# Kernel optimization log

Hardware: AMD Instinct MI355X
Metric: run time of the kernel (lower is better)

## Reference

```python
import jax, jax.numpy as jnp
import numpy as np

B, T, D = 4, 1024, 2048
H = 32
HD = D // H  # 64
NEG = -1e9


def setup_inputs() -> dict:
    key = jax.random.key(0)
    ks = jax.random.split(key, 12)
    s = 0.02
    x = jax.random.normal(ks[0], (B, T, D), dtype=jnp.float32)
    # additive causal mask [1, 1, T, T]
    causal = jnp.tril(jnp.ones((T, T), dtype=bool))
    attention_mask = jnp.where(causal, 0.0, NEG).astype(jnp.float32)[None, None]
    cache = jnp.zeros((B, 2, T, H, HD), dtype=jnp.float32)
    return {
        "x": x,
        "attention_mask": attention_mask,
        "cache": cache,
        "cache_update_index": 0,
        "Wq": jax.random.normal(ks[1], (D, D), jnp.float32) * s,
        "bq": jnp.zeros((D,), jnp.float32),
        "Wk": jax.random.normal(ks[2], (D, D), jnp.float32) * s,
        "bk": jnp.zeros((D,), jnp.float32),
        "Wv": jax.random.normal(ks[3], (D, D), jnp.float32) * s,
        "bv": jnp.zeros((D,), jnp.float32),
        "Wo": jax.random.normal(ks[4], (D, D), jnp.float32) * s,
        "bo": jnp.zeros((D,), jnp.float32),
    }


def _split_heads(t):
    b, s, _ = t.shape
    return t.reshape(b, s, H, HD).transpose(0, 2, 1, 3)  # (B,H,T,HD)


def reference(x, attention_mask, cache, cache_update_index, Wq, bq, Wk, bk, Wv, bv, Wo, bo):
    q = _split_heads(x @ Wq + bq)  # (B,H,T,HD)
    k = _split_heads(x @ Wk + bk)
    v = _split_heads(x @ Wv + bv)

    # update KV cache (cache layout: [B, 2, max_len, H, HD])
    k_for_cache = k.transpose(0, 2, 1, 3)  # (B,T,H,HD)
    v_for_cache = v.transpose(0, 2, 1, 3)
    idx = (0, cache_update_index, 0, 0)
    k_cache = jax.lax.dynamic_update_slice(cache[:, 0], k_for_cache, idx)
    v_cache = jax.lax.dynamic_update_slice(cache[:, 1], v_for_cache, idx)
    new_cache = jnp.stack([k_cache, v_cache], axis=1)
    k = k_cache.transpose(0, 2, 1, 3)  # (B,H,S,HD)
    v = v_cache.transpose(0, 2, 1, 3)

    scale = jnp.asarray(HD, q.dtype) ** -0.5
    scores = jnp.einsum("bhqd,bhkd->bhqk", q, k) * scale + attention_mask.astype(q.dtype)
    attn = jax.nn.softmax(scores, axis=-1)
    ctx = jnp.einsum("bhqk,bhkd->bhqd", attn, v)  # (B,H,T,HD)
    merged = ctx.transpose(0, 2, 1, 3).reshape(x.shape[0], x.shape[1], D)
    out = merged @ Wo + bo
    return out, new_cache
```

## Files before the change

### kernel.cpp

```cpp
#include <hip/hip_runtime.h>
#include <hip/hip_bf16.h>
#include <stdint.h>


typedef __hip_bfloat16 bf16;
typedef short s16x8 __attribute__((ext_vector_type(8)));
typedef float f32x4 __attribute__((ext_vector_type(4)));

#define T_SEQ   1024
#define D_MODEL 2048

__device__ inline unsigned short f2b(float f) {
    bf16 h = __float2bfloat16(f);
    return *(unsigned short*)&h;
}

typedef __attribute__((address_space(1))) const void gas_void;
typedef __attribute__((address_space(3))) void las_void;

__device__ inline void gl2lds16(const void* g, void* l) {
    __builtin_amdgcn_global_load_lds((gas_void*)g, (las_void*)l, 16, 0, 0);
}

__global__ __launch_bounds__(256)
void cvtx_kernel(const float* __restrict__ x, unsigned short* __restrict__ xb)
{
    const size_t i = ((size_t)blockIdx.x * 256 + threadIdx.x) * 8;
    float4 a = *(const float4*)(x + i);
    float4 b = *(const float4*)(x + i + 4);
    union { uint4 u; unsigned short s[8]; } p;
    p.s[0] = f2b(a.x); p.s[1] = f2b(a.y); p.s[2] = f2b(a.z); p.s[3] = f2b(a.w);
    p.s[4] = f2b(b.x); p.s[5] = f2b(b.y); p.s[6] = f2b(b.z); p.s[7] = f2b(b.w);
    *(uint4*)(xb + i) = p.u;
}

__global__ __launch_bounds__(256)
void wtrans_kernel(const float* __restrict__ W, unsigned short* __restrict__ Wt)
{
    __shared__ float tile[64][65];
    const int tid = threadIdx.x;
    const int k0 = blockIdx.y * 64, n0 = blockIdx.x * 64;

    const int rr = tid >> 4, cc = (tid & 15) * 4;
    #pragma unroll
    for (int i = 0; i < 4; ++i) {
        float4 v = *(const float4*)(W + (size_t)(k0 + rr + i * 16) * D_MODEL + n0 + cc);
        tile[rr + i * 16][cc]     = v.x;
        tile[rr + i * 16][cc + 1] = v.y;
        tile[rr + i * 16][cc + 2] = v.z;
        tile[rr + i * 16][cc + 3] = v.w;
    }
    __syncthreads();

    const int nr = tid >> 3, kc = (tid & 7) * 8;
    #pragma unroll
    for (int i = 0; i < 2; ++i) {
        const int n = nr + i * 32;
        union { uint4 u; unsigned short s[8]; } p;
        #pragma unroll
        for (int j = 0; j < 8; ++j) p.s[j] = f2b(tile[kc + j][n]);
        *(uint4*)(Wt + (size_t)(n0 + n) * D_MODEL + k0 + kc) = p.u;
    }
}

template<int MODE>
__global__ __launch_bounds__(256)
void gemm128_kernel(const unsigned short* __restrict__ A,
                    const unsigned short* __restrict__ Bt,
                    const float* __restrict__ bias,
                    float* __restrict__ out,
                    int slot, const int* __restrict__ idxp)
{
    __shared__ __align__(16) unsigned short As[128 * 32];
    __shared__ __align__(16) unsigned short Bs[128 * 32];

    const int tid  = threadIdx.x;
    const int wave = tid >> 6;
    const int lane = tid & 63;
    const int quad = lane >> 4;
    const int l15  = lane & 15;
    const int wm   = wave >> 1;
    const int wn   = wave & 1;
    const int m0   = blockIdx.y * 128;
    const int n0   = blockIdx.x * 128;

    const int ca   = wave * 2;
    const int rowc = lane >> 2;
    const int kofs = (lane & 3) * 8;

    const unsigned short* aG = A  + (size_t)(m0 + ca * 16 + rowc) * D_MODEL + kofs;
    const unsigned short* bG = Bt + (size_t)(n0 + ca * 16 + rowc) * D_MODEL + kofs;
    unsigned short* aL = As + ca * 512;
    unsigned short* bL = Bs + ca * 512;

    f32x4 acc[4][4];
    #pragma unroll
    for (int mi = 0; mi < 4; ++mi)
        #pragma unroll
        for (int ni = 0; ni < 4; ++ni) acc[mi][ni] = f32x4{0.f, 0.f, 0.f, 0.f};

    for (int k0 = 0; k0 < D_MODEL; k0 += 32) {
        gl2lds16(aG + k0,                aL);
        gl2lds16(aG + k0 + 16 * D_MODEL, aL + 512);
        gl2lds16(bG + k0,                bL);
        gl2lds16(bG + k0 + 16 * D_MODEL, bL + 512);
        __syncthreads();

        s16x8 af[4], bfr[4];
        #pragma unroll
        for (int mi = 0; mi < 4; ++mi)
            af[mi] = *(const s16x8*)(As + (wm * 64 + mi * 16 + l15) * 32 + quad * 8);
        #pragma unroll
        for (int ni = 0; ni < 4; ++ni)
            bfr[ni] = *(const s16x8*)(Bs + (wn * 64 + ni * 16 + l15) * 32 + quad * 8);
        #pragma unroll
        for (int mi = 0; mi < 4; ++mi)
            #pragma unroll
            for (int ni = 0; ni < 4; ++ni)
                acc[mi][ni] = __builtin_amdgcn_mfma_f32_16x16x32_bf16(af[mi], bfr[ni], acc[mi][ni], 0, 0, 0);
        __syncthreads();
    }

    const int idx = (MODE == 1) ? idxp[0] : 0;
    #pragma unroll
    for (int ni = 0; ni < 4; ++ni) {
        const int col = n0 + wn * 64 + ni * 16 + l15;
        const float bv = bias[col];
        #pragma unroll
        for (int mi = 0; mi < 4; ++mi) {
            #pragma unroll
            for (int r = 0; r < 4; ++r) {
                const int m = m0 + wm * 64 + mi * 16 + quad * 4 + r;
                const float v = acc[mi][ni][r] + bv;
                if (MODE == 0) {
                    out[(size_t)m * D_MODEL + col] = v;
                } else if (MODE == 1) {
                    const int b  = m >> 10;
                    const int tt = ((m & 1023) + idx) & 1023;
                    out[((size_t)(b * 2 + slot) * T_SEQ + tt) * D_MODEL + col] = v;
                } else {
                    ((unsigned short*)out)[(size_t)m * D_MODEL + col] = f2b(v);
                }
            }
        }
    }
}

#define LDW 72

__global__ __launch_bounds__(256)
void attn_mfma_kernel(const unsigned short* __restrict__ q,
                      const float* __restrict__ cache,
                      unsigned short* __restrict__ ctx)
{
    __shared__ __align__(16) unsigned short Qs[64 * LDW];
    __shared__ __align__(16) unsigned short Ks[64 * LDW];
    __shared__ __align__(16) unsigned short Vt[64 * LDW];
    __shared__ __align__(16) unsigned short Ps[64 * LDW];

    const int tid  = threadIdx.x;
    const int wave = tid >> 6;
    const int lane = tid & 63;
    const int quad = lane >> 4;
    const int l15  = lane & 15;

    const int bh = blockIdx.x;
    const int b  = bh >> 5;
    const int h  = bh & 31;
    const int qt = 15 - blockIdx.y;

    const int srow = tid >> 2;
    const int part = tid & 3;

    const float* kbase = cache + ((size_t)(b * 2 + 0) * T_SEQ) * D_MODEL + h * 64;
    const float* vbase = cache + ((size_t)(b * 2 + 1) * T_SEQ) * D_MODEL + h * 64;

    {
        const uint4* qg = (const uint4*)(q + (size_t)(b * T_SEQ + qt * 64 + srow) * D_MODEL
                                           + h * 64 + part * 16);
        uint4 q0 = qg[0], q1 = qg[1];
        *(uint4*)(Qs + srow * LDW + part * 16)     = q0;
        *(uint4*)(Qs + srow * LDW + part * 16 + 8) = q1;
    }
    __syncthreads();

    const s16x8 qf0 = *(const s16x8*)(Qs + (wave * 16 + l15) * LDW + quad * 8);
    const s16x8 qf1 = *(const s16x8*)(Qs + (wave * 16 + l15) * LDW + 32 + quad * 8);

    f32x4 oacc[4];
    #pragma unroll
    for (int t = 0; t < 4; ++t) oacc[t] = f32x4{0.f, 0.f, 0.f, 0.f};
    float m_run[4] = {-1e30f, -1e30f, -1e30f, -1e30f};
    float l_run[4] = {0.f, 0.f, 0.f, 0.f};

    for (int kt = 0; kt <= qt; ++kt) {
        __syncthreads();

        {
            const float4* kg = (const float4*)(kbase + (size_t)(kt * 64 + srow) * D_MODEL + part * 16);
            const float4* vg = (const float4*)(vbase + (size_t)(kt * 64 + srow) * D_MODEL + part * 16);
            float4 k0 = kg[0], k1 = kg[1], k2 = kg[2], k3 = kg[3];
            float4 v0 = vg[0], v1 = vg[1], v2 = vg[2], v3 = vg[3];
            float kv[16] = {k0.x, k0.y, k0.z, k0.w, k1.x, k1.y, k1.z, k1.w,
                            k2.x, k2.y, k2.z, k2.w, k3.x, k3.y, k3.z, k3.w};
            float vv[16] = {v0.x, v0.y, v0.z, v0.w, v1.x, v1.y, v1.z, v1.w,
                            v2.x, v2.y, v2.z, v2.w, v3.x, v3.y, v3.z, v3.w};
            union { uint4 u; unsigned short s[8]; } p0, p1;
            #pragma unroll
            for (int i = 0; i < 8; ++i) { p0.s[i] = f2b(kv[i]); p1.s[i] = f2b(kv[8 + i]); }
            *(uint4*)(Ks + srow * LDW + part * 16)     = p0.u;
            *(uint4*)(Ks + srow * LDW + part * 16 + 8) = p1.u;
            #pragma unroll
            for (int j = 0; j < 16; ++j) Vt[(part * 16 + j) * LDW + srow] = f2b(vv[j]);
        }
        __syncthreads();

        f32x4 sacc[4];
        #pragma unroll
        for (int t = 0; t < 4; ++t) sacc[t] = f32x4{0.f, 0.f, 0.f, 0.f};
        #pragma unroll
        for (int t = 0; t < 4; ++t) {
            s16x8 kf0 = *(const s16x8*)(Ks + (t * 16 + l15) * LDW + quad * 8);
            s16x8 kf1 = *(const s16x8*)(Ks + (t * 16 + l15) * LDW + 32 + quad * 8);
            sacc[t] = __builtin_amdgcn_mfma_f32_16x16x32_bf16(qf0, kf0, sacc[t], 0, 0, 0);
            sacc[t] = __builtin_amdgcn_mfma_f32_16x16x32_bf16(qf1, kf1, sacc[t], 0, 0, 0);
        }
        #pragma unroll
        for (int t = 0; t < 4; ++t)
            #pragma unroll
            for (int r = 0; r < 4; ++r) sacc[t][r] *= 0.125f;

        if (kt == qt) {
            #pragma unroll
            for (int t = 0; t < 4; ++t) {
                const int keyl = t * 16 + l15;
                #pragma unroll
                for (int r = 0; r < 4; ++r) {
                    if (keyl > wave * 16 + quad * 4 + r) sacc[t][r] = -1e30f;
                }
            }
        }

        float rmax[4];
        #pragma unroll
        for (int r = 0; r < 4; ++r)
            rmax[r] = fmaxf(fmaxf(sacc[0][r], sacc[1][r]), fmaxf(sacc[2][r], sacc[3][r]));
        #pragma unroll
        for (int off = 1; off < 16; off <<= 1) {
            #pragma unroll
            for (int r = 0; r < 4; ++r) rmax[r] = fmaxf(rmax[r], __shfl_xor(rmax[r], off, 16));
        }
        float alpha[4];
        #pragma unroll
        for (int r = 0; r < 4; ++r) {
            const float mnew = fmaxf(m_run[r], rmax[r]);
            alpha[r] = __expf(m_run[r] - mnew);
            m_run[r] = mnew;
        }
        float rsum[4] = {0.f, 0.f, 0.f, 0.f};
        #pragma unroll
        for (int t = 0; t < 4; ++t) {
            #pragma unroll
            for (int r = 0; r < 4; ++r) {
                const float p = __expf(sacc[t][r] - m_run[r]);
                sacc[t][r] = p;
                rsum[r] += p;
            }
        }
        #pragma unroll
        for (int off = 1; off < 16; off <<= 1) {
            #pragma unroll
            for (int r = 0; r < 4; ++r) rsum[r] += __shfl_xor(rsum[r], off, 16);
        }
        #pragma unroll
        for (int r = 0; r < 4; ++r) l_run[r] = l_run[r] * alpha[r] + rsum[r];
        #pragma unroll
        for (int t = 0; t < 4; ++t) {
            #pragma unroll
            for (int r = 0; r < 4; ++r) oacc[t][r] *= alpha[r];
        }

        #pragma unroll
        for (int t = 0; t < 4; ++t) {
            #pragma unroll
            for (int r = 0; r < 4; ++r)
                Ps[(wave * 16 + quad * 4 + r) * LDW + t * 16 + l15] = f2b(sacc[t][r]);
        }

        s16x8 pf0 = *(const s16x8*)(Ps + (wave * 16 + l15) * LDW + quad * 8);
        s16x8 pf1 = *(const s16x8*)(Ps + (wave * 16 + l15) * LDW + 32 + quad * 8);
        #pragma unroll
        for (int t = 0; t < 4; ++t) {
            s16x8 vf0 = *(const s16x8*)(Vt + (t * 16 + l15) * LDW + quad * 8);
            s16x8 vf1 = *(const s16x8*)(Vt + (t * 16 + l15) * LDW + 32 + quad * 8);
            oacc[t] = __builtin_amdgcn_mfma_f32_16x16x32_bf16(pf0, vf0, oacc[t], 0, 0, 0);
            oacc[t] = __builtin_amdgcn_mfma_f32_16x16x32_bf16(pf1, vf1, oacc[t], 0, 0, 0);
        }
    }

    float invl[4];
    #pragma unroll
    for (int r = 0; r < 4; ++r) invl[r] = 1.0f / l_run[r];
    #pragma unroll
    for (int r = 0; r < 4; ++r) {
        const int qrow = qt * 64 + wave * 16 + quad * 4 + r;
        unsigned short* orow = ctx + (size_t)(b * T_SEQ + qrow) * D_MODEL + h * 64;
        #pragma unroll
        for (int t = 0; t < 4; ++t) orow[t * 16 + l15] = f2b(oacc[t][r] * invl[r]);
    }
}

extern "C" void kernel_launch(void* const* d_in, const int* in_sizes, int n_in,
                              void* d_out, int out_size, void* d_ws, size_t ws_size,
                              hipStream_t stream)
{
    const float* x    = (const float*)d_in[0];
    const int*   idxp = (const int*)d_in[3];
    const float* Wq   = (const float*)d_in[4];
    const float* bq   = (const float*)d_in[5];
    const float* Wk   = (const float*)d_in[6];
    const float* bk   = (const float*)d_in[7];
    const float* Wv   = (const float*)d_in[8];
    const float* bv   = (const float*)d_in[9];
    const float* Wo   = (const float*)d_in[10];
    const float* bo   = (const float*)d_in[11];

    float* out = (float*)d_out;
    unsigned short* xb = (unsigned short*)d_out;
    unsigned short* qb = (unsigned short*)d_out + (size_t)8 * 1024 * 1024;
    float* cacheOut    = out + (size_t)4 * T_SEQ * D_MODEL;

    unsigned short* WT   = (unsigned short*)d_ws;
    unsigned short* ctxb = (unsigned short*)d_ws + (size_t)4 * 1024 * 1024;

    const dim3 tb(256);
    const dim3 tg(32, 32);
    const dim3 gg(16, 32);

    cvtx_kernel<<<dim3(4096), tb, 0, stream>>>(x, xb);

    wtrans_kernel<<<tg, tb, 0, stream>>>(Wq, WT);
    gemm128_kernel<2><<<gg, tb, 0, stream>>>(xb, WT, bq, (float*)qb, 0, nullptr);

    wtrans_kernel<<<tg, tb, 0, stream>>>(Wk, WT);
    gemm128_kernel<1><<<gg, tb, 0, stream>>>(xb, WT, bk, cacheOut, 0, idxp);

    wtrans_kernel<<<tg, tb, 0, stream>>>(Wv, WT);
    gemm128_kernel<1><<<gg, tb, 0, stream>>>(xb, WT, bv, cacheOut, 1, idxp);

    attn_mfma_kernel<<<dim3(128, 16), tb, 0, stream>>>(qb, cacheOut, ctxb);

    wtrans_kernel<<<tg, tb, 0, stream>>>(Wo, WT);
    gemm128_kernel<0><<<gg, tb, 0, stream>>>(ctxb, WT, bo, out, 0, nullptr);
}
```

Baseline: 479.2 us.

## Fuse QKV projections into one GEMM and widen attention tiles to 128 queries

The three weight transposes are batched into one launch, and the Q, K and V projections become a single GEMM with N=6144. Its epilogue routes each column range to the Q buffer, which now has the 1/8 softmax scale folded in, or to the K/V cache. Attention blocks now hold 128 query rows in 8 waves, so each K/V tile load is shared by twice as many queries. Waves whose rows are fully masked skip the tile, and the P staging reuses the Q shared buffer. The output GEMM uses 128x64 tiles so more blocks cover the grid. This cuts launches and redundant K/V conversion traffic, but adds more complex epilogue branching and higher register and shared-memory use per block.

New measurement: 486.3 us. No clear change (+1.5%).

```diff
diff --git a/kernel.cpp b/kernel.cpp
--- a/kernel.cpp
+++ b/kernel.cpp
@@ -4,15 +4,16 @@
 
 
 typedef __hip_bfloat16 bf16;
+typedef unsigned short us;
 typedef short s16x8 __attribute__((ext_vector_type(8)));
 typedef float f32x4 __attribute__((ext_vector_type(4)));
 
 #define T_SEQ   1024
 #define D_MODEL 2048
 
-__device__ inline unsigned short f2b(float f) {
+__device__ inline us f2b(float f) {
     bf16 h = __float2bfloat16(f);
-    return *(unsigned short*)&h;
+    return *(us*)&h;
 }
 
 typedef __attribute__((address_space(1))) const void gas_void;
@@ -23,21 +24,26 @@
 }
 
 __global__ __launch_bounds__(256)
-void cvtx_kernel(const float* __restrict__ x, unsigned short* __restrict__ xb)
+void cvtx_kernel(const float* __restrict__ x, us* __restrict__ xb)
 {
     const size_t i = ((size_t)blockIdx.x * 256 + threadIdx.x) * 8;
     float4 a = *(const float4*)(x + i);
     float4 b = *(const float4*)(x + i + 4);
-    union { uint4 u; unsigned short s[8]; } p;
+    union { uint4 u; us s[8]; } p;
     p.s[0] = f2b(a.x); p.s[1] = f2b(a.y); p.s[2] = f2b(a.z); p.s[3] = f2b(a.w);
     p.s[4] = f2b(b.x); p.s[5] = f2b(b.y); p.s[6] = f2b(b.z); p.s[7] = f2b(b.w);
     *(uint4*)(xb + i) = p.u;
 }
 
 __global__ __launch_bounds__(256)
-void wtrans_kernel(const float* __restrict__ W, unsigned short* __restrict__ Wt)
+void wtrans_kernel(const float* __restrict__ W0, const float* __restrict__ W1,
+                   const float* __restrict__ W2, us* __restrict__ Wt)
 {
     __shared__ float tile[64][65];
+    const int z = blockIdx.z;
+    const float* W = (z == 0) ? W0 : (z == 1) ? W1 : W2;
+    us* dst = Wt + (size_t)z * D_MODEL * D_MODEL;
+
     const int tid = threadIdx.x;
     const int k0 = blockIdx.y * 64, n0 = blockIdx.x * 64;
 
@@ -56,23 +62,23 @@
     #pragma unroll
     for (int i = 0; i < 2; ++i) {
         const int n = nr + i * 32;
-        union { uint4 u; unsigned short s[8]; } p;
+        union { uint4 u; us s[8]; } p;
         #pragma unroll
         for (int j = 0; j < 8; ++j) p.s[j] = f2b(tile[kc + j][n]);
-        *(uint4*)(Wt + (size_t)(n0 + n) * D_MODEL + k0 + kc) = p.u;
-    }
-}
-
-template<int MODE>
+        *(uint4*)(dst + (size_t)(n0 + n) * D_MODEL + k0 + kc) = p.u;
+    }
+}
+
+template<int MODE, int NI>
 __global__ __launch_bounds__(256)
-void gemm128_kernel(const unsigned short* __restrict__ A,
-                    const unsigned short* __restrict__ Bt,
-                    const float* __restrict__ bias,
-                    float* __restrict__ out,
-                    int slot, const int* __restrict__ idxp)
-{
-    __shared__ __align__(16) unsigned short As[128 * 32];
-    __shared__ __align__(16) unsigned short Bs[128 * 32];
+void gemm_kernel(const us* __restrict__ A, const us* __restrict__ Bt,
+                 const float* __restrict__ b0, const float* __restrict__ b1,
+                 const float* __restrict__ b2,
+                 float* __restrict__ out0, float* __restrict__ out1,
+                 const int* __restrict__ idxp)
+{
+    __shared__ __align__(16) us As[128 * 32];
+    __shared__ __align__(16) us Bs[NI * 32 * 32];
 
     const int tid  = threadIdx.x;
     const int wave = tid >> 6;
@@ -82,50 +88,59 @@
     const int wm   = wave >> 1;
     const int wn   = wave & 1;
     const int m0   = blockIdx.y * 128;
-    const int n0   = blockIdx.x * 128;
-
+    const int n0   = blockIdx.x * (NI * 32);
+
+    constexpr int BCH = NI / 2;
     const int ca   = wave * 2;
     const int rowc = lane >> 2;
     const int kofs = (lane & 3) * 8;
 
-    const unsigned short* aG = A  + (size_t)(m0 + ca * 16 + rowc) * D_MODEL + kofs;
-    const unsigned short* bG = Bt + (size_t)(n0 + ca * 16 + rowc) * D_MODEL + kofs;
-    unsigned short* aL = As + ca * 512;
-    unsigned short* bL = Bs + ca * 512;
-
-    f32x4 acc[4][4];
+    const us* aG = A  + (size_t)(m0 + ca * 16 + rowc) * D_MODEL + kofs;
+    const us* bG = Bt + (size_t)(n0 + wave * BCH * 16 + rowc) * D_MODEL + kofs;
+    us* aL = As + ca * 512;
+    us* bL = Bs + wave * BCH * 512;
+
+    f32x4 acc[4][NI];
     #pragma unroll
     for (int mi = 0; mi < 4; ++mi)
         #pragma unroll
-        for (int ni = 0; ni < 4; ++ni) acc[mi][ni] = f32x4{0.f, 0.f, 0.f, 0.f};
+        for (int ni = 0; ni < NI; ++ni) acc[mi][ni] = f32x4{0.f, 0.f, 0.f, 0.f};
 
     for (int k0 = 0; k0 < D_MODEL; k0 += 32) {
         gl2lds16(aG + k0,                aL);
         gl2lds16(aG + k0 + 16 * D_MODEL, aL + 512);
-        gl2lds16(bG + k0,                bL);
-        gl2lds16(bG + k0 + 16 * D_MODEL, bL + 512);
+        if constexpr (BCH == 2) {
+            gl2lds16(bG + k0,                bL);
+            gl2lds16(bG + k0 + 16 * D_MODEL, bL + 512);
+        } else {
+            gl2lds16(bG + k0, bL);
+        }
         __syncthreads();
 
-        s16x8 af[4], bfr[4];
+        s16x8 af[4], bfr[NI];
         #pragma unroll
         for (int mi = 0; mi < 4; ++mi)
             af[mi] = *(const s16x8*)(As + (wm * 64 + mi * 16 + l15) * 32 + quad * 8);
         #pragma unroll
-        for (int ni = 0; ni < 4; ++ni)
-            bfr[ni] = *(const s16x8*)(Bs + (wn * 64 + ni * 16 + l15) * 32 + quad * 8);
+        for (int ni = 0; ni < NI; ++ni)
+            bfr[ni] = *(const s16x8*)(Bs + (wn * NI * 16 + ni * 16 + l15) * 32 + quad * 8);
         #pragma unroll
         for (int mi = 0; mi < 4; ++mi)
             #pragma unroll
-            for (int ni = 0; ni < 4; ++ni)
+            for (int ni = 0; ni < NI; ++ni)
                 acc[mi][ni] = __builtin_amdgcn_mfma_f32_16x16x32_bf16(af[mi], bfr[ni], acc[mi][ni], 0, 0, 0);
         __syncthreads();
     }
 
-    const int idx = (MODE == 1) ? idxp[0] : 0;
-    #pragma unroll
-    for (int ni = 0; ni < 4; ++ni) {
-        const int col = n0 + wn * 64 + ni * 16 + l15;
-        const float bv = bias[col];
+    const int reg = (MODE == 3) ? (n0 >> 11) : 0;
+    const float* bias = (MODE == 3) ? (reg == 0 ? b0 : (reg == 1 ? b1 : b2)) : b0;
+    const int idx = (MODE == 3 && reg > 0) ? idxp[0] : 0;
+
+    #pragma unroll
+    for (int ni = 0; ni < NI; ++ni) {
+        const int col = n0 + wn * NI * 16 + ni * 16 + l15;
+        const int cl  = col & (D_MODEL - 1);
+        const float bv = bias[cl];
         #pragma unroll
         for (int mi = 0; mi < 4; ++mi) {
             #pragma unroll
@@ -133,30 +148,31 @@
                 const int m = m0 + wm * 64 + mi * 16 + quad * 4 + r;
                 const float v = acc[mi][ni][r] + bv;
                 if (MODE == 0) {
-                    out[(size_t)m * D_MODEL + col] = v;
-                } else if (MODE == 1) {
-                    const int b  = m >> 10;
-                    const int tt = ((m & 1023) + idx) & 1023;
-                    out[((size_t)(b * 2 + slot) * T_SEQ + tt) * D_MODEL + col] = v;
+                    out0[(size_t)m * D_MODEL + cl] = v;
                 } else {
-                    ((unsigned short*)out)[(size_t)m * D_MODEL + col] = f2b(v);
+                    if (reg == 0) {
+                        ((us*)out0)[(size_t)m * D_MODEL + cl] = f2b(v * 0.125f);
+                    } else {
+                        const int b  = m >> 10;
+                        const int tt = ((m & 1023) + idx) & 1023;
+                        out1[((size_t)(b * 2 + (reg - 1)) * T_SEQ + tt) * D_MODEL + cl] = v;
+                    }
                 }
             }
         }
     }
 }
 
-#define LDW 72
-
-__global__ __launch_bounds__(256)
-void attn_mfma_kernel(const unsigned short* __restrict__ q,
-                      const float* __restrict__ cache,
-                      unsigned short* __restrict__ ctx)
-{
-    __shared__ __align__(16) unsigned short Qs[64 * LDW];
-    __shared__ __align__(16) unsigned short Ks[64 * LDW];
-    __shared__ __align__(16) unsigned short Vt[64 * LDW];
-    __shared__ __align__(16) unsigned short Ps[64 * LDW];
+#define LDW  72
+#define LDWV 70
+
+__global__ __launch_bounds__(512, 6)
+void attn_mfma_kernel(const us* __restrict__ q, const float* __restrict__ cache,
+                      us* __restrict__ ctx)
+{
+    __shared__ __align__(16) us Qs[128 * LDW];
+    __shared__ __align__(16) us Ks[64 * LDW];
+    __shared__ __align__(16) us Vt[64 * LDWV];
 
     const int tid  = threadIdx.x;
     const int wave = tid >> 6;
@@ -167,20 +183,19 @@
     const int bh = blockIdx.x;
     const int b  = bh >> 5;
     const int h  = bh & 31;
-    const int qt = 15 - blockIdx.y;
-
-    const int srow = tid >> 2;
-    const int part = tid & 3;
+    const int qt = 7 - blockIdx.y;
 
     const float* kbase = cache + ((size_t)(b * 2 + 0) * T_SEQ) * D_MODEL + h * 64;
     const float* vbase = cache + ((size_t)(b * 2 + 1) * T_SEQ) * D_MODEL + h * 64;
 
     {
-        const uint4* qg = (const uint4*)(q + (size_t)(b * T_SEQ + qt * 64 + srow) * D_MODEL
-                                           + h * 64 + part * 16);
+        const int qrow = tid >> 2;
+        const int qp   = tid & 3;
+        const uint4* qg = (const uint4*)(q + (size_t)(b * T_SEQ + qt * 128 + qrow) * D_MODEL
+                                           + h * 64 + qp * 16);
         uint4 q0 = qg[0], q1 = qg[1];
-        *(uint4*)(Qs + srow * LDW + part * 16)     = q0;
-        *(uint4*)(Qs + srow * LDW + part * 16 + 8) = q1;
+        *(uint4*)(Qs + qrow * LDW + qp * 16)     = q0;
+        *(uint4*)(Qs + qrow * LDW + qp * 16 + 8) = q1;
     }
     __syncthreads();
 
@@ -193,108 +208,116 @@
     float m_run[4] = {-1e30f, -1e30f, -1e30f, -1e30f};
     float l_run[4] = {0.f, 0.f, 0.f, 0.f};
 
-    for (int kt = 0; kt <= qt; ++kt) {
+    const int nkt = 2 * qt + 2;
+
+    const int ksrow = tid >> 3;
+    const int kp8   = tid & 7;
+    const int vs    = tid >> 4;
+    const int vp4   = tid & 15;
+
+    for (int kt = 0; kt < nkt; ++kt) {
         __syncthreads();
 
         {
-            const float4* kg = (const float4*)(kbase + (size_t)(kt * 64 + srow) * D_MODEL + part * 16);
-            const float4* vg = (const float4*)(vbase + (size_t)(kt * 64 + srow) * D_MODEL + part * 16);
-            float4 k0 = kg[0], k1 = kg[1], k2 = kg[2], k3 = kg[3];
-            float4 v0 = vg[0], v1 = vg[1], v2 = vg[2], v3 = vg[3];
-            float kv[16] = {k0.x, k0.y, k0.z, k0.w, k1.x, k1.y, k1.z, k1.w,
-                            k2.x, k2.y, k2.z, k2.w, k3.x, k3.y, k3.z, k3.w};
-            float vv[16] = {v0.x, v0.y, v0.z, v0.w, v1.x, v1.y, v1.z, v1.w,
-                            v2.x, v2.y, v2.z, v2.w, v3.x, v3.y, v3.z, v3.w};
-            union { uint4 u; unsigned short s[8]; } p0, p1;
-            #pragma unroll
-            for (int i = 0; i < 8; ++i) { p0.s[i] = f2b(kv[i]); p1.s[i] = f2b(kv[8 + i]); }
-            *(uint4*)(Ks + srow * LDW + part * 16)     = p0.u;
-            *(uint4*)(Ks + srow * LDW + part * 16 + 8) = p1.u;
-            #pragma unroll
-            for (int j = 0; j < 16; ++j) Vt[(part * 16 + j) * LDW + srow] = f2b(vv[j]);
+            const float4* kg = (const float4*)(kbase + (size_t)(kt * 64 + ksrow) * D_MODEL + kp8 * 8);
+            float4 k0 = kg[0], k1 = kg[1];
+            union { uint4 u; us s[8]; } p;
+            p.s[0] = f2b(k0.x); p.s[1] = f2b(k0.y); p.s[2] = f2b(k0.z); p.s[3] = f2b(k0.w);
+            p.s[4] = f2b(k1.x); p.s[5] = f2b(k1.y); p.s[6] = f2b(k1.z); p.s[7] = f2b(k1.w);
+            *(uint4*)(Ks + ksrow * LDW + kp8 * 8) = p.u;
+        }
+        {
+            const float4 a = *(const float4*)(vbase + (size_t)(kt * 64 + 2 * vs) * D_MODEL + vp4 * 4);
+            const float4 c = *(const float4*)(vbase + (size_t)(kt * 64 + 2 * vs + 1) * D_MODEL + vp4 * 4);
+            const float av[4] = {a.x, a.y, a.z, a.w};
+            const float cv[4] = {c.x, c.y, c.z, c.w};
+            #pragma unroll
+            for (int j = 0; j < 4; ++j) {
+                ushort2 w; w.x = f2b(av[j]); w.y = f2b(cv[j]);
+                *(ushort2*)(Vt + (vp4 * 4 + j) * LDWV + 2 * vs) = w;
+            }
         }
         __syncthreads();
 
-        f32x4 sacc[4];
-        #pragma unroll
-        for (int t = 0; t < 4; ++t) sacc[t] = f32x4{0.f, 0.f, 0.f, 0.f};
-        #pragma unroll
-        for (int t = 0; t < 4; ++t) {
-            s16x8 kf0 = *(const s16x8*)(Ks + (t * 16 + l15) * LDW + quad * 8);
-            s16x8 kf1 = *(const s16x8*)(Ks + (t * 16 + l15) * LDW + 32 + quad * 8);
-            sacc[t] = __builtin_amdgcn_mfma_f32_16x16x32_bf16(qf0, kf0, sacc[t], 0, 0, 0);
-            sacc[t] = __builtin_amdgcn_mfma_f32_16x16x32_bf16(qf1, kf1, sacc[t], 0, 0, 0);
-        }
-        #pragma unroll
-        for (int t = 0; t < 4; ++t)
-            #pragma unroll
-            for (int r = 0; r < 4; ++r) sacc[t][r] *= 0.125f;
-
-        if (kt == qt) {
-            #pragma unroll
-            for (int t = 0; t < 4; ++t) {
-                const int keyl = t * 16 + l15;
+        const int kbr = kt * 64 - qt * 128;
+        if (kbr < wave * 16 + 16) {
+            f32x4 sacc[4];
+            #pragma unroll
+            for (int t = 0; t < 4; ++t) sacc[t] = f32x4{0.f, 0.f, 0.f, 0.f};
+            #pragma unroll
+            for (int t = 0; t < 4; ++t) {
+                s16x8 kf0 = *(const s16x8*)(Ks + (t * 16 + l15) * LDW + quad * 8);
+                s16x8 kf1 = *(const s16x8*)(Ks + (t * 16 + l15) * LDW + 32 + quad * 8);
+                sacc[t] = __builtin_amdgcn_mfma_f32_16x16x32_bf16(qf0, kf0, sacc[t], 0, 0, 0);
+                sacc[t] = __builtin_amdgcn_mfma_f32_16x16x32_bf16(qf1, kf1, sacc[t], 0, 0, 0);
+            }
+
+            if (kbr + 63 > wave * 16) {
+                #pragma unroll
+                for (int t = 0; t < 4; ++t) {
+                    const int keyl = kbr + t * 16 + l15;
+                    #pragma unroll
+                    for (int r = 0; r < 4; ++r) {
+                        if (keyl > wave * 16 + quad * 4 + r) sacc[t][r] = -1e30f;
+                    }
+                }
+            }
+
+            float rmax[4];
+            #pragma unroll
+            for (int r = 0; r < 4; ++r)
+                rmax[r] = fmaxf(fmaxf(sacc[0][r], sacc[1][r]), fmaxf(sacc[2][r], sacc[3][r]));
+            #pragma unroll
+            for (int off = 1; off < 16; off <<= 1) {
+                #pragma unroll
+                for (int r = 0; r < 4; ++r) rmax[r] = fmaxf(rmax[r], __shfl_xor(rmax[r], off, 16));
+            }
+            float alpha[4];
+            #pragma unroll
+            for (int r = 0; r < 4; ++r) {
+                const float mnew = fmaxf(m_run[r], rmax[r]);
+                alpha[r] = __expf(m_run[r] - mnew);
+                m_run[r] = mnew;
+            }
+            float rsum[4] = {0.f, 0.f, 0.f, 0.f};
+            #pragma unroll
+            for (int t = 0; t < 4; ++t) {
                 #pragma unroll
                 for (int r = 0; r < 4; ++r) {
-                    if (keyl > wave * 16 + quad * 4 + r) sacc[t][r] = -1e30f;
+                    const float p = __expf(sacc[t][r] - m_run[r]);
+                    sacc[t][r] = p;
+                    rsum[r] += p;
                 }
             }
-        }
-
-        float rmax[4];
-        #pragma unroll
-        for (int r = 0; r < 4; ++r)
-            rmax[r] = fmaxf(fmaxf(sacc[0][r], sacc[1][r]), fmaxf(sacc[2][r], sacc[3][r]));
-        #pragma unroll
-        for (int off = 1; off < 16; off <<= 1) {
-            #pragma unroll
-            for (int r = 0; r < 4; ++r) rmax[r] = fmaxf(rmax[r], __shfl_xor(rmax[r], off, 16));
-        }
-        float alpha[4];
-        #pragma unroll
-        for (int r = 0; r < 4; ++r) {
-            const float mnew = fmaxf(m_run[r], rmax[r]);
-            alpha[r] = __expf(m_run[r] - mnew);
-            m_run[r] = mnew;
-        }
-        float rsum[4] = {0.f, 0.f, 0.f, 0.f};
-        #pragma unroll
-        for (int t = 0; t < 4; ++t) {
-            #pragma unroll
-            for (int r = 0; r < 4; ++r) {
-                const float p = __expf(sacc[t][r] - m_run[r]);
-                sacc[t][r] = p;
-                rsum[r] += p;
-            }
-        }
-        #pragma unroll
-        for (int off = 1; off < 16; off <<= 1) {
-            #pragma unroll
-            for (int r = 0; r < 4; ++r) rsum[r] += __shfl_xor(rsum[r], off, 16);
-        }
-        #pragma unroll
-        for (int r = 0; r < 4; ++r) l_run[r] = l_run[r] * alpha[r] + rsum[r];
-        #pragma unroll
-        for (int t = 0; t < 4; ++t) {
-            #pragma unroll
-            for (int r = 0; r < 4; ++r) oacc[t][r] *= alpha[r];
-        }
-
-        #pragma unroll
-        for (int t = 0; t < 4; ++t) {
-            #pragma unroll
-            for (int r = 0; r < 4; ++r)
-                Ps[(wave * 16 + quad * 4 + r) * LDW + t * 16 + l15] = f2b(sacc[t][r]);
-        }
-
-        s16x8 pf0 = *(const s16x8*)(Ps + (wave * 16 + l15) * LDW + quad * 8);
-        s16x8 pf1 = *(const s16x8*)(Ps + (wave * 16 + l15) * LDW + 32 + quad * 8);
-        #pragma unroll
-        for (int t = 0; t < 4; ++t) {
-            s16x8 vf0 = *(const s16x8*)(Vt + (t * 16 + l15) * LDW + quad * 8);
-            s16x8 vf1 = *(const s16x8*)(Vt + (t * 16 + l15) * LDW + 32 + quad * 8);
-            oacc[t] = __builtin_amdgcn_mfma_f32_16x16x32_bf16(pf0, vf0, oacc[t], 0, 0, 0);
-            oacc[t] = __builtin_amdgcn_mfma_f32_16x16x32_bf16(pf1, vf1, oacc[t], 0, 0, 0);
+            #pragma unroll
+            for (int off = 1; off < 16; off <<= 1) {
+                #pragma unroll
+                for (int r = 0; r < 4; ++r) rsum[r] += __shfl_xor(rsum[r], off, 16);
+            }
+            #pragma unroll
+            for (int r = 0; r < 4; ++r) l_run[r] = l_run[r] * alpha[r] + rsum[r];
+            #pragma unroll
+            for (int t = 0; t < 4; ++t) {
+                #pragma unroll
+                for (int r = 0; r < 4; ++r) oacc[t][r] *= alpha[r];
+            }
+
+            #pragma unroll
+            for (int t = 0; t < 4; ++t) {
+                #pragma unroll
+                for (int r = 0; r < 4; ++r)
+                    Qs[(wave * 16 + quad * 4 + r) * LDW + t * 16 + l15] = f2b(sacc[t][r]);
+            }
+
+            s16x8 pf0 = *(const s16x8*)(Qs + (wave * 16 + l15) * LDW + quad * 8);
+            s16x8 pf1 = *(const s16x8*)(Qs + (wave * 16 + l15) * LDW + 32 + quad * 8);
+            #pragma unroll
+            for (int t = 0; t < 4; ++t) {
+                s16x8 vf0 = *(const s16x8*)(Vt + (t * 16 + l15) * LDWV + quad * 8);
+                s16x8 vf1 = *(const s16x8*)(Vt + (t * 16 + l15) * LDWV + 32 + quad * 8);
+                oacc[t] = __builtin_amdgcn_mfma_f32_16x16x32_bf16(pf0, vf0, oacc[t], 0, 0, 0);
+                oacc[t] = __builtin_amdgcn_mfma_f32_16x16x32_bf16(pf1, vf1, oacc[t], 0, 0, 0);
+            }
         }
     }
 
@@ -303,8 +326,8 @@
     for (int r = 0; r < 4; ++r) invl[r] = 1.0f / l_run[r];
     #pragma unroll
     for (int r = 0; r < 4; ++r) {
-        const int qrow = qt * 64 + wave * 16 + quad * 4 + r;
-        unsigned short* orow = ctx + (size_t)(b * T_SEQ + qrow) * D_MODEL + h * 64;
+        const int qrow = qt * 128 + wave * 16 + quad * 4 + r;
+        us* orow = ctx + (size_t)(b * T_SEQ + qrow) * D_MODEL + h * 64;
         #pragma unroll
         for (int t = 0; t < 4; ++t) orow[t * 16 + l15] = f2b(oacc[t][r] * invl[r]);
     }
@@ -325,31 +348,27 @@
     const float* Wo   = (const float*)d_in[10];
     const float* bo   = (const float*)d_in[11];
 
-    float* out = (float*)d_out;
-    unsigned short* xb = (unsigned short*)d_out;
-    unsigned short* qb = (unsigned short*)d_out + (size_t)8 * 1024 * 1024;
-    float* cacheOut    = out + (size_t)4 * T_SEQ * D_MODEL;
-
-    unsigned short* WT   = (unsigned short*)d_ws;
-    unsigned short* ctxb = (unsigned short*)d_ws + (size_t)4 * 1024 * 1024;
+    float* out      = (float*)d_out;
+    us*    xb       = (us*)d_out;
+    us*    qb       = (us*)d_out + (size_t)8 * 1024 * 1024;
+    float* cacheOut = out + (size_t)4 * T_SEQ * D_MODEL;
+
+    us* WT3  = (us*)d_ws;
+    us* WTo  = (us*)d_ws;
+    us* ctxb = (us*)d_ws + (size_t)4 * 1024 * 1024;
 
     const dim3 tb(256);
-    const dim3 tg(32, 32);
-    const dim3 gg(16, 32);
 
     cvtx_kernel<<<dim3(4096), tb, 0, stream>>>(x, xb);
-
-    wtrans_kernel<<<tg, tb, 0, stream>>>(Wq, WT);
-    gemm128_kernel<2><<<gg, tb, 0, stream>>>(xb, WT, bq, (float*)qb, 0, nullptr);
-
-    wtrans_kernel<<<tg, tb, 0, stream>>>(Wk, WT);
-    gemm128_kernel<1><<<gg, tb, 0, stream>>>(xb, WT, bk, cacheOut, 0, idxp);
-
-    wtrans_kernel<<<tg, tb, 0, stream>>>(Wv, WT);
-    gemm128_kernel<1><<<gg, tb, 0, stream>>>(xb, WT, bv, cacheOut, 1, idxp);
-
-    attn_mfma_kernel<<<dim3(128, 16), tb, 0, stream>>>(qb, cacheOut, ctxb);
-
-    wtrans_kernel<<<tg, tb, 0, stream>>>(Wo, WT);
-    gemm128_kernel<0><<<gg, tb, 0, stream>>>(ctxb, WT, bo, out, 0, nullptr);
-}
+    wtrans_kernel<<<dim3(32, 32, 3), tb, 0, stream>>>(Wq, Wk, Wv, WT3);
+
+    gemm_kernel<3, 4><<<dim3(48, 32), tb, 0, stream>>>(
+        xb, WT3, bq, bk, bv, (float*)qb, cacheOut, idxp);
+
+    wtrans_kernel<<<dim3(32, 32, 1), tb, 0, stream>>>(Wo, Wo, Wo, WTo);
+
+    attn_mfma_kernel<<<dim3(128, 8), dim3(512), 0, stream>>>(qb, cacheOut, ctxb);
+
+    gemm_kernel<0, 2><<<dim3(32, 32), tb, 0, stream>>>(
+        ctxb, WTo, bo, nullptr, nullptr, out, nullptr, nullptr);
+}
```
